# Kernel tuning notes

Hardware: AMD Instinct MI355X
Metric: run time of the kernel (lower is better)

## Reference

```python
import jax, jax.numpy as jnp
import numpy as np

B, NPTS = 2, 60000
NX, NY = 256, 256
PCR0, PCR1 = -32.0, -32.0
PS0, PS1 = 0.25, 0.25
MAXPP = 32      # max points per pillar
MAXP = 12000    # max pillars
C = 64          # lidar_channels
SENT = NX * NY  # sentinel pillar id (> any valid id)
NEG = -1e9
EPS = 1e-5


def setup_inputs():
    key = jax.random.key(0)
    ks = jax.random.split(key, 16)
    xy = jax.random.uniform(ks[0], (B, NPTS, 2), minval=-34.0, maxval=34.0)
    z = jax.random.uniform(ks[1], (B, NPTS, 1), minval=-3.0, maxval=1.0)
    ir = jax.random.uniform(ks[2], (B, NPTS, 2))
    pts = jnp.concatenate([xy, z, ir], axis=-1).astype(jnp.float32)
    mask = jax.random.uniform(ks[3], (B, NPTS)) < 0.98

    def lin(k, i, o):
        return (jax.random.normal(k, (i, o)) / np.sqrt(i)).astype(jnp.float32)

    inp = {"lidar_points": pts, "lidar_mask": mask,
           "w1": lin(ks[4], 10, 64), "b1": 0.01 * jax.random.normal(ks[5], (64,), jnp.float32),
           "g1": jnp.ones(64, jnp.float32), "be1": jnp.zeros(64, jnp.float32),
           "w2": lin(ks[6], 64, 64), "b2": 0.01 * jax.random.normal(ks[7], (64,), jnp.float32),
           "g2": jnp.ones(64, jnp.float32), "be2": jnp.zeros(64, jnp.float32)}
    for i, n in enumerate(["1", "2", "3"]):
        inp["cw" + n] = (jax.random.normal(ks[8 + i], (64, 64, 3, 3)) / np.sqrt(64 * 9)).astype(jnp.float32)
        inp["cb" + n] = 0.01 * jax.random.normal(ks[11 + i], (64,), jnp.float32)
        inp["cg" + n] = jnp.ones(64, jnp.float32)
        inp["cbe" + n] = jnp.zeros(64, jnp.float32)
    return inp


def bn1d(x, g, b):  # training-mode BN over rows (biased var), matches torch BatchNorm1d forward
    m = x.mean(0)
    v = ((x - m) ** 2).mean(0)
    return (x - m) * jax.lax.rsqrt(v + EPS) * g + b


def bn2d(x, g, b):  # training-mode BN over (N,H,W) per channel
    m = x.mean((0, 2, 3), keepdims=True)
    v = ((x - m) ** 2).mean((0, 2, 3), keepdims=True)
    return (x - m) * jax.lax.rsqrt(v + EPS) * g[None, :, None, None] + b[None, :, None, None]


def conv3(x, w, b):
    y = jax.lax.conv_general_dilated(x, w, (1, 1), 'SAME',
                                     dimension_numbers=('NCHW', 'OIHW', 'NCHW'))
    return y + b[None, :, None, None]


def pillarize(pts, msk):
    """pts: (N,5) xyzir, msk: (N,) bool -> padded pillar tensors (fixed shapes)."""
    n = pts.shape[0]
    ix = jnp.clip(((pts[:, 0] - PCR0) / PS0).astype(jnp.int32), 0, NX - 1)
    iy = jnp.clip(((pts[:, 1] - PCR1) / PS1).astype(jnp.int32), 0, NY - 1)
    pid = jnp.where(msk, iy * NX + ix, SENT)
    # sorted unique ids; keep the first (smallest) MAXP, like torch.unique + truncation
    spid = jnp.sort(pid)
    is_new = jnp.concatenate([jnp.array([True]), spid[1:] != spid[:-1]])
    urank = jnp.cumsum(is_new) - 1
    dest = jnp.where(is_new & (urank < MAXP) & (spid < SENT), urank, MAXP)
    uids = jnp.full((MAXP + 1,), SENT, dtype=pid.dtype).at[dest].set(spid)[:MAXP]  # ascending, SENT-padded
    inv = jnp.clip(jnp.searchsorted(uids, pid), 0, MAXP - 1)
    valid = (uids[inv] == pid) & (pid < SENT)
    # rank of each point within its pillar, in original point order (stable sort)
    seg = jnp.where(valid, inv, MAXP)
    order = jnp.argsort(seg)  # stable
    sseg = seg[order]
    pos = jnp.arange(n)
    first = jnp.concatenate([jnp.array([True]), sseg[1:] != sseg[:-1]])
    start = jax.lax.cummax(jnp.where(first, pos, 0))
    rank = jnp.zeros(n, jnp.int32).at[order].set((pos - start).astype(jnp.int32))
    keep = valid & (rank < MAXPP)  # first MAXPP points per pillar (matches truncation-then-mean)
    seg2 = jnp.where(keep, inv, MAXP)  # dump slot = MAXP
    cnt = jnp.zeros(MAXP + 1, pts.dtype).at[seg2].add(1.0)
    sums = jnp.zeros((MAXP + 1, 3), pts.dtype).at[seg2].add(jnp.where(keep[:, None], pts[:, :3], 0.0))
    mean = sums / jnp.maximum(cnt, 1.0)[:, None]
    ctr = mean[seg2]  # per-point pillar centroid (over kept points)
    gx = PCR0 + ((pid % NX).astype(pts.dtype) + 0.5) * PS0
    gy = PCR1 + ((pid // NX).astype(pts.dtype) + 0.5) * PS1
    aug = jnp.concatenate([pts, pts[:, :3] - ctr, gx[:, None], gy[:, None]], axis=1)  # (N,10)
    rk = jnp.minimum(rank, MAXPP - 1)
    pf = jnp.zeros((MAXP + 1, MAXPP, 10), pts.dtype).at[seg2, rk].set(
        jnp.where(keep[:, None], aug, 0.0))[:MAXP]
    pm = jnp.zeros((MAXP + 1, MAXPP), bool).at[seg2, rk].set(keep)[:MAXP]
    pvalid = uids < SENT
    coords = jnp.where(pvalid[:, None], jnp.stack([uids % NX, uids // NX], axis=-1), 0)
    return pf, pm, coords, pvalid


def pillar_net(pf, pm, w1, b1, g1, be1, w2, b2, g2, be2):
    npil, pp, ci = pf.shape
    x = pf.reshape(npil * pp, ci) @ w1 + b1
    x = jax.nn.relu(bn1d(x, g1, be1))
    x = x @ w2 + b2
    x = jax.nn.relu(bn1d(x, g2, be2))
    x = x.reshape(npil, pp, -1)
    x = jnp.where(pm[:, :, None], x, NEG)
    return x.max(axis=1)  # (npil, C)


def reference(lidar_points, lidar_mask, w1, b1, g1, be1, w2, b2, g2, be2,
              cw1, cb1, cg1, cbe1, cw2, cb2, cg2, cbe2, cw3, cb3, cg3, cbe3):
    pf, pm, coords, pvalid = jax.vmap(pillarize)(lidar_points, lidar_mask)
    # pillar net is applied per batch element in the original loop -> per-sample BN stats
    feat = jax.vmap(lambda a, m: pillar_net(a, m, w1, b1, g1, be1, w2, b2, g2, be2))(pf, pm)
    lin = coords[..., 1] * NX + coords[..., 0]          # (B, MAXP)
    f = jnp.where(pvalid[..., None], feat, 0.0)          # padded pillars contribute nothing
    bev = jax.vmap(lambda l, ff: jnp.zeros((NY * NX, C), ff.dtype).at[l].add(ff))(lin, f)
    bev = bev.reshape(-1, NY, NX, C).transpose(0, 3, 1, 2)  # (B,C,NY,NX)
    x = jax.nn.relu(bn2d(conv3(bev, cw1, cb1), cg1, cbe1))
    x = jax.nn.relu(bn2d(conv3(x, cw2, cb2), cg2, cbe2))
    x = jax.nn.relu(bn2d(conv3(x, cw3, cb3), cg3, cbe3))
    return x
```

## Files before the change

### kernel.cpp

```cpp
#include <hip/hip_runtime.h>

#define NPTS 60000
#define NXG 256
#define NCELL 65536
#define MAXP 12000
#define MAXPP 32
#define NROWS (MAXP*MAXPP)

typedef float f32x32 __attribute__((ext_vector_type(32)));
typedef float f32x4  __attribute__((ext_vector_type(4)));
typedef short s16x8  __attribute__((ext_vector_type(8)));

__device__ __forceinline__ short to_bf16(float f){
  unsigned u = __float_as_uint(f);
  unsigned r = (u + 0x7FFFu + ((u>>16)&1u)) >> 16;
  return (short)r;
}
__device__ __forceinline__ unsigned mapf(float f){
  unsigned u = __float_as_uint(f);
  return (u & 0x80000000u) ? ~u : (u | 0x80000000u);
}
__device__ __forceinline__ float unmapf(unsigned u){
  unsigned b = (u & 0x80000000u) ? (u ^ 0x80000000u) : ~u;
  return __uint_as_float(b);
}

__global__ __launch_bounds__(256) void prep(uint4* __restrict__ p1, size_t n1,
                                            uint4* __restrict__ p2, size_t n2,
                                            const float* __restrict__ w0, const float* __restrict__ w1,
                                            const float* __restrict__ w2, short* __restrict__ wh,
                                            const float* __restrict__ mw1, const float* __restrict__ mw2,
                                            short* __restrict__ w1h, short* __restrict__ w2h,
                                            uint4* __restrict__ fmn, size_t nfmn){
  size_t idx = (size_t)blockIdx.x*256 + threadIdx.x;
  size_t stride = (size_t)gridDim.x*256;
  const uint4 z = make_uint4(0,0,0,0);
  const uint4 ff = make_uint4(0xFFFFFFFFu,0xFFFFFFFFu,0xFFFFFFFFu,0xFFFFFFFFu);
  for (size_t k=idx; k<n1; k+=stride) p1[k]=z;
  for (size_t k=idx; k<n2; k+=stride) p2[k]=z;
  for (size_t k=idx; k<nfmn; k+=stride) fmn[k]=ff;
  for (size_t k=idx; k<3*36864; k+=stride){
    int l = (int)(k / 36864), r = (int)(k - (size_t)l*36864);
    const float* w = (l==0)? w0 : ((l==1)? w1 : w2);
    int ic = r & 63, oc = (r>>6)&63, tap = r>>12;
    wh[k] = to_bf16(w[(oc*64+ic)*9 + tap]);
  }
  for (size_t k=idx; k<2048; k+=stride){
    int kk = (int)(k>>6), oc = (int)(k&63);
    w1h[k] = (kk<10) ? to_bf16(mw1[kk*64+oc]) : (short)0;
  }
  for (size_t k=idx; k<4096; k+=stride)
    w2h[k] = to_bf16(mw2[k]);
}

__global__ void compute_pid(const float* __restrict__ pts, const void* __restrict__ maskp,
                            int* __restrict__ pid, int* __restrict__ ccnt){
  __shared__ int cf32, cbig;
  if (threadIdx.x==0){ cf32=0; cbig=0; }
  __syncthreads();
  {
    int lf=0, lb=0;
    const unsigned* mu = (const unsigned*)maskp;
    for (int k=0;k<4;k++){
      unsigned x = mu[threadIdx.x*4+k];
      if (x==0x3f800000u) lf++;
      else if (x>1u) lb++;
    }
    if (lf) atomicAdd(&cf32, lf);
    if (lb) atomicAdd(&cbig, lb);
  }
  __syncthreads();
  int mode = (cf32>64) ? 2 : ((cbig>0) ? 1 : 0);
  int i = blockIdx.x*blockDim.x + threadIdx.x;
  if (i>=NPTS) return;
  int b = blockIdx.y;
  int gi = b*NPTS+i;
  bool m;
  if (mode==0)      m = ((const int*)maskp)[gi]!=0;
  else if (mode==1) m = ((const unsigned char*)maskp)[gi]!=0;
  else              m = ((const float*)maskp)[gi]!=0.f;
  int cell = -1;
  if (m){
    float x = pts[(size_t)gi*5+0], y = pts[(size_t)gi*5+1];
    int ix = (int)((x - (-32.0f)) / 0.25f);
    ix = ix<0?0:(ix>255?255:ix);
    int iy = (int)((y - (-32.0f)) / 0.25f);
    iy = iy<0?0:(iy>255?255:iy);
    cell = iy*NXG + ix;
    atomicAdd(&ccnt[b*NCELL+cell], 1);
  }
  pid[gi] = cell;
}

__global__ __launch_bounds__(256) void scan_a(const int* __restrict__ ccnt,
                                              int2* __restrict__ bpart){
  int b = blockIdx.y, blk = blockIdx.x, t = threadIdx.x;
  int4 v = *(const int4*)&ccnt[b*NCELL + blk*1024 + t*4];
  int occ = (v.x>0)+(v.y>0)+(v.z>0)+(v.w>0);
  int cnt = v.x+v.y+v.z+v.w;
  #pragma unroll
  for (int off=32; off>0; off>>=1){
    occ += __shfl_xor(occ, off, 64);
    cnt += __shfl_xor(cnt, off, 64);
  }
  __shared__ int so[4], sc[4];
  int wv = t>>6, lane = t&63;
  if (lane==0){ so[wv]=occ; sc[wv]=cnt; }
  __syncthreads();
  if (t==0) bpart[b*64+blk] = make_int2(so[0]+so[1]+so[2]+so[3], sc[0]+sc[1]+sc[2]+sc[3]);
}

__global__ __launch_bounds__(256) void scan_b(const int* __restrict__ ccnt,
    const int2* __restrict__ bpart,
    int* __restrict__ crank, int* __restrict__ cstart, int* __restrict__ pcell,
    int* __restrict__ misc, int* __restrict__ heavy){
  __shared__ int swo[4], swc[4], sk[4];
  __shared__ int bo_, bc_;
  int b = blockIdx.y, blk = blockIdx.x, t = threadIdx.x;
  int wv = t>>6, lane = t&63;
  if (t < 64){
    int2 p = bpart[b*64+t];
    int po = (t<blk)? p.x : 0;
    int pc = (t<blk)? p.y : 0;
    int to = p.x;
    int tc = p.y;
    #pragma unroll
    for (int off=32; off>0; off>>=1){
      po += __shfl_xor(po, off, 64);
      pc += __shfl_xor(pc, off, 64);
      to += __shfl_xor(to, off, 64);
      tc += __shfl_xor(tc, off, 64);
    }
    if (t==0){
      bo_ = po; bc_ = pc;
      if (blk==0){
        misc[1+b] = (to < MAXP) ? to : MAXP;
        misc[5+b] = tc;
      }
    }
  }
  int4 v = *(const int4*)&ccnt[b*NCELL + blk*1024 + t*4];
  int occ = (v.x>0)+(v.y>0)+(v.z>0)+(v.w>0);
  int cnt = v.x+v.y+v.z+v.w;
  int io = occ, ic = cnt;
  #pragma unroll
  for (int off=1; off<64; off<<=1){
    int ao = __shfl_up(io, off, 64);
    int ac = __shfl_up(ic, off, 64);
    if (lane >= off){ io += ao; ic += ac; }
  }
  if (lane==63){ swo[wv]=io; swc[wv]=ic; }
  __syncthreads();
  int wvo=0, wvc=0;
  #pragma unroll
  for (int w2=0; w2<4; w2++){
    if (w2<wv){ wvo += swo[w2]; wvc += swc[w2]; }
  }
  int eo = bo_ + wvo + io - occ;
  int ec = bc_ + wvc + ic - cnt;
  int kept = 0;
  int cellb = blk*1024 + t*4;
  int vv[4] = {v.x,v.y,v.z,v.w};
  #pragma unroll
  for (int j=0;j<4;j++){
    int c = cellb+j; int val = vv[j];
    if (val>0){
      crank[b*NCELL+c]=eo; cstart[b*NCELL+c]=ec;
      if (eo<MAXP){
        pcell[b*MAXP+eo]=c;
        kept += (val<MAXPP)? val : MAXPP;
        if (val>MAXPP){
          int hi = atomicAdd(&heavy[b],1);
          if (hi<64) heavy[2 + b*64 + hi] = c;
        }
      }
      eo++; ec+=val;
    }
  }
  #pragma unroll
  for (int off=32; off>0; off>>=1) kept += __shfl_xor(kept, off, 64);
  if (lane==0) sk[wv]=kept;
  __syncthreads();
  if (t==0) atomicAdd(&misc[3+b], sk[0]+sk[1]+sk[2]+sk[3]);
}

__global__ void scatter_cpts(const float* __restrict__ pts, const int* __restrict__ pid,
    const int* __restrict__ ccnt, const int* __restrict__ crank, const int* __restrict__ cstart,
    int* __restrict__ ctmp, int* __restrict__ plist,
    float* __restrict__ cpts, float* __restrict__ psum){
  int i = blockIdx.x*blockDim.x + threadIdx.x;
  if (i>=NPTS) return;
  int b = blockIdx.y;
  int gi = b*NPTS+i;
  int cell = pid[gi];
  if (cell<0) return;
  int bc = b*NCELL+cell;
  int pos = cstart[bc] + atomicAdd(&ctmp[bc],1);
  plist[b*NPTS+pos] = i;
  int cnt = ccnt[bc], r = crank[bc];
  int rid = (r<MAXP && cnt<=MAXPP) ? r : -1;
  const float* qp = &pts[(size_t)gi*5];
  float x=qp[0], y=qp[1], z=qp[2], i1=qp[3], i2=qp[4];
  float gx = -32.0f + ((float)(cell&255)+0.5f)*0.25f;
  float gy = -32.0f + ((float)(cell>>8)+0.5f)*0.25f;
  float4* cp = (float4*)&cpts[(size_t)(b*NPTS+pos)*12];
  cp[0] = make_float4(x,y,z,i1);
  cp[1] = make_float4(i2,gx,gy,__int_as_float(rid));
  if (rid>=0){
    float* s = &psum[(size_t)(b*MAXP+rid)*4];
    atomicAdd(s+0,x); atomicAdd(s+1,y); atomicAdd(s+2,z); atomicAdd(s+3,1.f);
  }
}

__global__ void heavy_select(const float* __restrict__ pts,
    const int* __restrict__ ccnt, const int* __restrict__ crank,
    const int* __restrict__ cstart, const int* __restrict__ plist,
    const int* __restrict__ heavy, float* __restrict__ cpts, float* __restrict__ psum){
  int b = blockIdx.y;
  int hn = heavy[b]; if (hn>64) hn=64;
  if ((int)blockIdx.x >= hn) return;
  int cell = heavy[2 + b*64 + blockIdx.x];
  int bc = b*NCELL+cell;
  int cnt = ccnt[bc], start = cstart[bc], pr = crank[bc];
  for (int e=threadIdx.x; e<cnt; e+=blockDim.x){
    int pe = plist[b*NPTS+start+e];
    int rank=0;
    for (int k=0;k<cnt;k++) rank += (plist[b*NPTS+start+k] < pe);
    if (rank<MAXPP && pr<MAXP){
      cpts[(size_t)(b*NPTS+start+e)*12 + 7] = __int_as_float(pr);
      const float* qp = &pts[(size_t)(b*NPTS+pe)*5];
      float* s = &psum[(size_t)(b*MAXP+pr)*4];
      atomicAdd(s+0,qp[0]); atomicAdd(s+1,qp[1]); atomicAdd(s+2,qp[2]); atomicAdd(s+3,1.f);
    }
  }
}

#define MM_ACC(K,V) { if ((K)<32) m0[(K)&31]+=(V); else if ((K)<64) m1[((K)-32)&31]+=(V); else m2+=(V); }
__global__ __launch_bounds__(256) void moments(float* __restrict__ cpts,
    const float* __restrict__ psum, const int* __restrict__ misc,
    float* __restrict__ lstat){
  int b = blockIdx.y;
  int n = misc[5+b];
  f32x32 m0, m1; float m2 = 0.f;
  #pragma unroll
  for (int j=0;j<32;j++){ m0[j]=0.f; m1[j]=0.f; }
  for (int pos = blockIdx.x*256+threadIdx.x; pos<n; pos += gridDim.x*256){
    float4* cp = (float4*)&cpts[(size_t)(b*NPTS+pos)*12];
    float4 f1 = cp[0], f2 = cp[1];
    int rid = __float_as_int(f2.w);
    if (rid<0) continue;
    float4 mc = *(const float4*)&psum[(size_t)(b*MAXP+rid)*4];
    float inv = 1.f/fmaxf(mc.w,1.f);
    float dx = f1.x-mc.x*inv, dy = f1.y-mc.y*inv, dz = f1.z-mc.z*inv;
    cp[2] = make_float4(dx,dy,dz,0.f);
    float aug[10] = {f1.x,f1.y,f1.z,f1.w,f2.x, dx,dy,dz, f2.y,f2.z};
    #pragma unroll
    for (int d=0; d<10; d++){
      #pragma unroll
      for (int e=d; e<10; e++){
        const int k = d*10 - d*(d-1)/2 + (e-d);
        MM_ACC(k, aug[d]*aug[e]);
      }
      const int kl = 55+d;
      MM_ACC(kl, aug[d]);
    }
  }
  int lane = threadIdx.x & 63;
  int rep = ((blockIdx.x*256+threadIdx.x)>>6) & 15;
  float* dst = &lstat[(size_t)(rep*2+b)*65];
  #pragma unroll
  for (int j=0;j<32;j++){
    float v = m0[j];
    #pragma unroll
    for (int off=32; off>0; off>>=1) v += __shfl_xor(v, off, 64);
    if (lane==0) atomicAdd(&dst[j], v);
  }
  #pragma unroll
  for (int j=0;j<32;j++){
    float v = m1[j];
    #pragma unroll
    for (int off=32; off>0; off>>=1) v += __shfl_xor(v, off, 64);
    if (lane==0) atomicAdd(&dst[32+j], v);
  }
  {
    float v = m2;
    #pragma unroll
    for (int off=32; off>0; off>>=1) v += __shfl_xor(v, off, 64);
    if (lane==0) atomicAdd(&dst[64], v);
  }
}

#define MFMA16(A,B,C) __builtin_amdgcn_mfma_f32_16x16x32_bf16(A,B,C,0,0,0)

__global__ __launch_bounds__(256) void point_mlp(const float* __restrict__ cpts,
    const int* __restrict__ misc,
    const float* __restrict__ w1, const float* __restrict__ b1,
    const float* __restrict__ g1, const float* __restrict__ be1,
    const short* __restrict__ w1h, const short* __restrict__ w2h,
    const float* __restrict__ lstat, float* __restrict__ l2stat,
    unsigned* __restrict__ fmxU, unsigned* __restrict__ fmnU){
  __shared__ float sM[65];
  __shared__ float sBN1[128];
  __shared__ short zT[4][16*72];
  const int b = blockIdx.y;
  const int t = threadIdx.x;
  for (int e=t; e<65; e+=256){
    float s=0.f;
    for (int r=0;r<16;r++) s += lstat[(size_t)(r*2+b)*65+e];
    sM[e]=s;
  }
  __syncthreads();
  if (t < 64){
    int c = t;
    float wcol[10];
    #pragma unroll
    for (int d=0;d<10;d++) wcol[d] = w1[d*64+c];
    float b1c = b1[c];
    float nk = (float)misc[3+b];
    const float N = (float)NROWS;
    float pad = N - nk;
    float lw = 0.f;
    #pragma unroll
    for (int d=0;d<10;d++) lw += sM[55+d]*wcol[d];
    float s = nk*b1c + lw;
    float qq = nk*b1c*b1c + 2.f*b1c*lw;
    #pragma unroll
    for (int d=0; d<10; d++){
      #pragma unroll
      for (int e=d; e<10; e++){
        float m = sM[d*10 - d*(d-1)/2 + (e-d)];
        qq += ((d==e)?1.f:2.f)*m*wcol[d]*wcol[e];
      }
    }
    float St = s + pad*b1c;
    float Qt = qq + pad*b1c*b1c;
    float mu = St/N;
    float var = fmaxf(Qt/N - mu*mu, 0.f);
    float sc = g1[c]*rsqrtf(var+1e-5f);
    float sh = be1[c]-mu*sc;
    sBN1[c]=sc; sBN1[64+c]=b1c*sc+sh;
  }
  __syncthreads();
  const int lane = t & 63, wv = t >> 6;
  const int colx = lane & 15;
  const int kq = lane >> 4, kb = kq*8;
  s16x8 w1f0, w1f1, w1f2, w1f3;
  s16x8 a2f0, a2f1, a2f2, a2f3;
  s16x8 b2f0, b2f1, b2f2, b2f3;
  #pragma unroll
  for (int j=0;j<8;j++){
    w1f0[j]=w1h[(kb+j)*64 +  0+colx]; w1f1[j]=w1h[(kb+j)*64 + 16+colx];
    w1f2[j]=w1h[(kb+j)*64 + 32+colx]; w1f3[j]=w1h[(kb+j)*64 + 48+colx];
    a2f0[j]=w2h[(kb+j)*64 +  0+colx]; a2f1[j]=w2h[(kb+j)*64 + 16+colx];
    a2f2[j]=w2h[(kb+j)*64 + 32+colx]; a2f3[j]=w2h[(kb+j)*64 + 48+colx];
    b2f0[j]=w2h[(32+kb+j)*64 +  0+colx]; b2f1[j]=w2h[(32+kb+j)*64 + 16+colx];
    b2f2[j]=w2h[(32+kb+j)*64 + 32+colx]; b2f3[j]=w2h[(32+kb+j)*64 + 48+colx];
  }
  float sc1v0=sBN1[colx],    sh1v0=sBN1[64+colx];
  float sc1v1=sBN1[16+colx], sh1v1=sBN1[80+colx];
  float sc1v2=sBN1[32+colx], sh1v2=sBN1[96+colx];
  float sc1v3=sBN1[48+colx], sh1v3=sBN1[112+colx];
  const int n = misc[5+b];
  const int ntiles = (n+15)>>4;
  short* myZ = zT[wv];
  f32x4 s24={0.f,0.f,0.f,0.f}, q24=s24;
  for (int tile = blockIdx.x*4 + wv; tile < ntiles; tile += gridDim.x*4){
    int pos0 = tile*16;
    int pos = pos0 + colx;
    float aug[10];
    #pragma unroll
    for (int d=0;d<10;d++) aug[d]=0.f;
    if (pos < n){
      const float4* cp = (const float4*)&cpts[(size_t)(b*NPTS+pos)*12];
      float4 f1 = cp[0], f2 = cp[1], f3 = cp[2];
      aug[0]=f1.x; aug[1]=f1.y; aug[2]=f1.z; aug[3]=f1.w; aug[4]=f2.x;
      aug[5]=f3.x; aug[6]=f3.y; aug[7]=f3.z;
      aug[8]=f2.y; aug[9]=f2.z;
    }
    s16x8 af;
    #pragma unroll
    for (int j=0;j<8;j++){
      float v = 0.f;
      if (kq==0) v = aug[j];
      else if (kq==1 && j<2) v = aug[8+j];
      af[j] = to_bf16(v);
    }
    f32x4 y0={0.f,0.f,0.f,0.f}, y1=y0, y2=y0, y3=y0;
    y0 = MFMA16(af, w1f0, y0);
    y1 = MFMA16(af, w1f1, y1);
    y2 = MFMA16(af, w1f2, y2);
    y3 = MFMA16(af, w1f3, y3);
    #pragma unroll
    for (int m=0;m<4;m++){
      int pr = (kq*4+m)*72;
      myZ[pr +  0+colx] = to_bf16(fmaxf(y0[m]*sc1v0+sh1v0, 0.f));
      myZ[pr + 16+colx] = to_bf16(fmaxf(y1[m]*sc1v1+sh1v1, 0.f));
      myZ[pr + 32+colx] = to_bf16(fmaxf(y2[m]*sc1v2+sh1v2, 0.f));
      myZ[pr + 48+colx] = to_bf16(fmaxf(y3[m]*sc1v3+sh1v3, 0.f));
    }
    s16x8 az0 = *(const s16x8*)&myZ[colx*72 + kb];
    s16x8 az1 = *(const s16x8*)&myZ[colx*72 + 32 + kb];
    f32x4 t0={0.f,0.f,0.f,0.f}, t1=t0, t2=t0, t3=t0;
    t0 = MFMA16(az0, a2f0, t0); t0 = MFMA16(az1, b2f0, t0);
    t1 = MFMA16(az0, a2f1, t1); t1 = MFMA16(az1, b2f1, t1);
    t2 = MFMA16(az0, a2f2, t2); t2 = MFMA16(az1, b2f2, t2);
    t3 = MFMA16(az0, a2f3, t3); t3 = MFMA16(az1, b2f3, t3);
    int cur = -1;
    f32x4 tmx={-1e30f,-1e30f,-1e30f,-1e30f}, tmn={1e30f,1e30f,1e30f,1e30f};
    #pragma unroll
    for (int m=0;m<4;m++){
      int pm = pos0 + kq*4 + m;
      int rid = -1;
      if (pm < n) rid = __float_as_int(cpts[(size_t)(b*NPTS+pm)*12 + 7]);
      if (rid != cur){
        if (cur >= 0){
          size_t base = (size_t)(b*MAXP+cur)*64;
          atomicMax(&fmxU[base+ 0+colx], mapf(tmx[0]));
          atomicMax(&fmxU[base+16+colx], mapf(tmx[1]));
          atomicMax(&fmxU[base+32+colx], mapf(tmx[2]));
          atomicMax(&fmxU[base+48+colx], mapf(tmx[3]));
          atomicMin(&fmnU[base+ 0+colx], mapf(tmn[0]));
          atomicMin(&fmnU[base+16+colx], mapf(tmn[1]));
          atomicMin(&fmnU[base+32+colx], mapf(tmn[2]));
          atomicMin(&fmnU[base+48+colx], mapf(tmn[3]));
        }
        cur = rid;
        tmx[0]=-1e30f; tmx[1]=-1e30f; tmx[2]=-1e30f; tmx[3]=-1e30f;
        tmn[0]= 1e30f; tmn[1]= 1e30f; tmn[2]= 1e30f; tmn[3]= 1e30f;
      }
      if (rid >= 0){
        float v0=t0[m], v1=t1[m], v2=t2[m], v3=t3[m];
        tmx[0]=fmaxf(tmx[0],v0); tmn[0]=fminf(tmn[0],v0);
        tmx[1]=fmaxf(tmx[1],v1); tmn[1]=fminf(tmn[1],v1);
        tmx[2]=fmaxf(tmx[2],v2); tmn[2]=fminf(tmn[2],v2);
        tmx[3]=fmaxf(tmx[3],v3); tmn[3]=fminf(tmn[3],v3);
        s24[0]+=v0; q24[0]+=v0*v0;
        s24[1]+=v1; q24[1]+=v1*v1;
        s24[2]+=v2; q24[2]+=v2*v2;
        s24[3]+=v3; q24[3]+=v3*v3;
      }
    }
    if (cur >= 0){
      size_t base = (size_t)(b*MAXP+cur)*64;
      atomicMax(&fmxU[base+ 0+colx], mapf(tmx[0]));
      atomicMax(&fmxU[base+16+colx], mapf(tmx[1]));
      atomicMax(&fmxU[base+32+colx], mapf(tmx[2]));
      atomicMax(&fmxU[base+48+colx], mapf(tmx[3]));
      atomicMin(&fmnU[base+ 0+colx], mapf(tmn[0]));
      atomicMin(&fmnU[base+16+colx], mapf(tmn[1]));
      atomicMin(&fmnU[base+32+colx], mapf(tmn[2]));
      atomicMin(&fmnU[base+48+colx], mapf(tmn[3]));
    }
  }
  int rep = (blockIdx.x*4 + wv) & 15;
  float* L = &l2stat[(size_t)((rep*2+b)*2+0)*64];
  atomicAdd(&L[ 0+colx], s24[0]);
  atomicAdd(&L[16+colx], s24[1]);
  atomicAdd(&L[32+colx], s24[2]);
  atomicAdd(&L[48+colx], s24[3]);
  float* Q = &l2stat[(size_t)((rep*2+b)*2+1)*64];
  atomicAdd(&Q[ 0+colx], q24[0]);
  atomicAdd(&Q[16+colx], q24[1]);
  atomicAdd(&Q[32+colx], q24[2]);
  atomicAdd(&Q[48+colx], q24[3]);
}

__global__ __launch_bounds__(256) void scatter_bev(
    const float* __restrict__ w1, const float* __restrict__ b1,
    const float* __restrict__ g1, const float* __restrict__ be1,
    const float* __restrict__ w2, const float* __restrict__ b2,
    const float* __restrict__ g2, const float* __restrict__ be2,
    const float* __restrict__ lstat, const float* __restrict__ l2stat,
    const unsigned* __restrict__ fmxU, const unsigned* __restrict__ fmnU,
    const int* __restrict__ pcell, const int* __restrict__ misc,
    short* __restrict__ bevh){
  __shared__ float M[65];
  __shared__ float z0s[64];
  __shared__ float sBN2[128];
  const int b = blockIdx.y;
  for (int e=threadIdx.x; e<65; e+=256){
    float s=0.f;
    for (int r=0;r<16;r++) s += lstat[(size_t)(r*2+b)*65+e];
    M[e]=s;
  }
  __syncthreads();
  if (threadIdx.x < 64){
    int c = threadIdx.x;
    float wcol[10];
    #pragma unroll
    for (int d=0;d<10;d++) wcol[d] = w1[d*64+c];
    float b1c = b1[c];
    float nk = (float)misc[3+b];
    const float N = (float)NROWS;
    float pad = N - nk;
    float lw = 0.f;
    #pragma unroll
    for (int d=0;d<10;d++) lw += M[55+d]*wcol[d];
    float s = nk*b1c + lw;
    float qq = nk*b1c*b1c + 2.f*b1c*lw;
    #pragma unroll
    for (int d=0; d<10; d++){
      #pragma unroll
      for (int e=d; e<10; e++){
        float m = M[d*10 - d*(d-1)/2 + (e-d)];
        qq += ((d==e)?1.f:2.f)*m*wcol[d]*wcol[e];
      }
    }
    float St = s + pad*b1c;
    float Qt = qq + pad*b1c*b1c;
    float mu = St/N;
    float var = fmaxf(Qt/N - mu*mu, 0.f);
    float sc1 = g1[c]*rsqrtf(var+1e-5f);
    float sh1 = be1[c]-mu*sc1;
    z0s[c] = fmaxf(b1c*sc1+sh1, 0.f);
  }
  __syncthreads();
  if (threadIdx.x < 64){
    int c = threadIdx.x;
    float nk = (float)misc[3+b];
    const float N = (float)NROWS;
    float pad = N - nk;
    float t0 = b2[c];
    for (int i2=0;i2<64;i2++) t0 += z0s[i2]*w2[(size_t)i2*64+c];
    float s2 = pad*t0, q2 = pad*t0*t0;
    for (int r=0;r<16;r++){
      s2 += l2stat[(size_t)((r*2+b)*2+0)*64+c];
      q2 += l2stat[(size_t)((r*2+b)*2+1)*64+c];
    }
    float m2 = s2/N;
    float v2 = fmaxf(q2/N - m2*m2, 0.f);
    float sc2 = g2[c]*rsqrtf(v2+1e-5f);
    sBN2[c]=sc2; sBN2[64+c]=be2[c]-m2*sc2;
  }
  __syncthreads();
  const int npil = misc[1+b];
  for (int tid = blockIdx.x*256+threadIdx.x; tid < 64*MAXP; tid += gridDim.x*256){
    int c = tid & 63;
    int p = tid >> 6;
    if (p >= npil) break;
    float sc2 = sBN2[c], sh2 = sBN2[64+c];
    size_t idx = (size_t)(b*MAXP+p)*64 + c;
    float tv = (sc2 >= 0.f) ? unmapf(fmxU[idx]) : unmapf(fmnU[idx]);
    float v = fmaxf(sc2*tv+sh2, 0.f);
    int cell = pcell[b*MAXP+p];
    bevh[((size_t)((b<<16) + cell))*64 + c] = to_bf16(v);
  }
}

__global__ __launch_bounds__(512,4) void conv_mfma(const short* __restrict__ xh,
    const short* __restrict__ wh, const float* __restrict__ bias,
    const float* __restrict__ pstat, const float* __restrict__ pg, const float* __restrict__ pbe,
    short* __restrict__ outh, float* __restrict__ outf,
    float* __restrict__ stat){
  __shared__ short sX[324*40];
  __shared__ short sW[576*40];
  __shared__ float sBN[128];
  __shared__ float ss[64], sq[64];
  const int tX = blockIdx.x*16, tY = blockIdx.y*16;
  const int b = blockIdx.z;
  const int t = threadIdx.x;
  const int lane = t & 63, wv = t >> 6;
  const int colx = lane & 15;
  const int kb = (lane >> 4) * 8;
  const int ocb = (wv >> 2) * 32;
  const int ry  = (wv & 3) * 4;
  if (t < 64){ ss[t]=0.f; sq[t]=0.f; }
  if (t >= 64 && t < 128 && pstat){
    int c = t-64;
    const float n = 131072.f;
    float m = pstat[c]/n;
    float v = fmaxf(pstat[64+c]/n - m*m, 0.f);
    float sc = pg[c]*rsqrtf(v+1e-5f);
    sBN[c]=sc; sBN[64+c]=pbe[c]-m*sc;
  }

  f32x4 a00={0.f,0.f,0.f,0.f}, a01=a00, a02=a00, a03=a00;
  f32x4 a10=a00, a11=a00, a12=a00, a13=a00;

  for (int h=0; h<2; ++h){
    __syncthreads();
    for (int e=t; e<1296; e+=512){
      int px = e>>2, j = e&3;
      int yy = px/18, xx = px - yy*18;
      int gy = tY+yy-1, gx = tX+xx-1;
      uint4 v = make_uint4(0,0,0,0);
      if ((unsigned)gy<256u && (unsigned)gx<256u){
        v = *(const uint4*)&xh[((size_t)((b<<16) + (gy<<8) + gx))*64 + h*32 + j*8];
        if (pstat){
          unsigned arr[4] = {v.x, v.y, v.z, v.w};
          #pragma unroll
          for (int j2=0;j2<4;j2++){
            unsigned wrd = arr[j2];
            int ch = h*32 + j*8 + j2*2;
            float lo = __uint_as_float(wrd<<16);
            float hi = __uint_as_float(wrd & 0xffff0000u);
            lo = fmaxf(lo*sBN[ch]+sBN[64+ch], 0.f);
            hi = fmaxf(hi*sBN[ch+1]+sBN[64+ch+1], 0.f);
            arr[j2] = (unsigned)(unsigned short)to_bf16(lo) |
                      (((unsigned)(unsigned short)to_bf16(hi))<<16);
          }
          v = make_uint4(arr[0],arr[1],arr[2],arr[3]);
        }
      }
      *(uint4*)&sX[px*40 + j*8] = v;
    }
    for (int e=t; e<2304; e+=512){
      int row = e>>2, j = e&3;
      int tap = row>>6, oc = row&63;
      uint4 v = *(const uint4*)&wh[(size_t)tap*4096 + oc*64 + h*32 + j*8];
      *(uint4*)&sW[row*40 + j*8] = v;
    }
    __syncthreads();
    #pragma unroll
    for (int tap=0; tap<9; ++tap){
      const int dy = tap/3, dx = tap - dy*3;
      s16x8 wA = *(const s16x8*)&sW[(tap*64 + ocb +  0 + colx)*40 + kb];
      s16x8 wB = *(const s16x8*)&sW[(tap*64 + ocb + 16 + colx)*40 + kb];
      s16x8 x0 = *(const s16x8*)&sX[((ry+0+dy)*18 + colx+dx)*40 + kb];
      s16x8 x1 = *(const s16x8*)&sX[((ry+1+dy)*18 + colx+dx)*40 + kb];
      s16x8 x2 = *(const s16x8*)&sX[((ry+2+dy)*18 + colx+dx)*40 + kb];
      s16x8 x3 = *(const s16x8*)&sX[((ry+3+dy)*18 + colx+dx)*40 + kb];
      a00 = MFMA16(wA,x0,a00); a01 = MFMA16(wA,x1,a01);
      a02 = MFMA16(wA,x2,a02); a03 = MFMA16(wA,x3,a03);
      a10 = MFMA16(wB,x0,a10); a11 = MFMA16(wB,x1,a11);
      a12 = MFMA16(wB,x2,a12); a13 = MFMA16(wB,x3,a13);
    }
  }
  const int ocl = (lane>>4)*4;
  #define DOG(G, A0,A1,A2,A3) { \
    const int oc0g = ocb + G*16 + ocl; \
    float bj0=bias[oc0g], bj1=bias[oc0g+1], bj2=bias[oc0g+2], bj3=bias[oc0g+3]; \
    float v00=A0[0]+bj0, v01=A0[1]+bj1, v02=A0[2]+bj2, v03=A0[3]+bj3; \
    float v10=A1[0]+bj0, v11=A1[1]+bj1, v12=A1[2]+bj2, v13=A1[3]+bj3; \
    float v20=A2[0]+bj0, v21=A2[1]+bj1, v22=A2[2]+bj2, v23=A2[3]+bj3; \
    float v30=A3[0]+bj0, v31=A3[1]+bj1, v32=A3[2]+bj2, v33=A3[3]+bj3; \
    float s0=v00+v10+v20+v30, q0=v00*v00+v10*v10+v20*v20+v30*v30; \
    float s1=v01+v11+v21+v31, q1=v01*v01+v11*v11+v21*v21+v31*v31; \
    float s2=v02+v12+v22+v32, q2=v02*v02+v12*v12+v22*v22+v32*v32; \
    float s3=v03+v13+v23+v33, q3=v03*v03+v13*v13+v23*v23+v33*v33; \
    s0+=__shfl_xor(s0,1,64); s0+=__shfl_xor(s0,2,64); s0+=__shfl_xor(s0,4,64); s0+=__shfl_xor(s0,8,64); \
    q0+=__shfl_xor(q0,1,64); q0+=__shfl_xor(q0,2,64); q0+=__shfl_xor(q0,4,64); q0+=__shfl_xor(q0,8,64); \
    s1+=__shfl_xor(s1,1,64); s1+=__shfl_xor(s1,2,64); s1+=__shfl_xor(s1,4,64); s1+=__shfl_xor(s1,8,64); \
    q1+=__shfl_xor(q1,1,64); q1+=__shfl_xor(q1,2,64); q1+=__shfl_xor(q1,4,64); q1+=__shfl_xor(q1,8,64); \
    s2+=__shfl_xor(s2,1,64); s2+=__shfl_xor(s2,2,64); s2+=__shfl_xor(s2,4,64); s2+=__shfl_xor(s2,8,64); \
    q2+=__shfl_xor(q2,1,64); q2+=__shfl_xor(q2,2,64); q2+=__shfl_xor(q2,4,64); q2+=__shfl_xor(q2,8,64); \
    s3+=__shfl_xor(s3,1,64); s3+=__shfl_xor(s3,2,64); s3+=__shfl_xor(s3,4,64); s3+=__shfl_xor(s3,8,64); \
    q3+=__shfl_xor(q3,1,64); q3+=__shfl_xor(q3,2,64); q3+=__shfl_xor(q3,4,64); q3+=__shfl_xor(q3,8,64); \
    if (colx==0){ \
      atomicAdd(&ss[oc0g],s0);   atomicAdd(&sq[oc0g],q0); \
      atomicAdd(&ss[oc0g+1],s1); atomicAdd(&sq[oc0g+1],q1); \
      atomicAdd(&ss[oc0g+2],s2); atomicAdd(&sq[oc0g+2],q2); \
      atomicAdd(&ss[oc0g+3],s3); atomicAdd(&sq[oc0g+3],q3); \
    } \
    if (outh){ \
      size_t pb = (size_t)((b<<16) + tX + colx); \
      *(short4*)&outh[(pb + ((tY+ry+0)<<8))*64 + oc0g] = make_short4(to_bf16(v00),to_bf16(v01),to_bf16(v02),to_bf16(v03)); \
      *(short4*)&outh[(pb + ((tY+ry+1)<<8))*64 + oc0g] = make_short4(to_bf16(v10),to_bf16(v11),to_bf16(v12),to_bf16(v13)); \
      *(short4*)&outh[(pb + ((tY+ry+2)<<8))*64 + oc0g] = make_short4(to_bf16(v20),to_bf16(v21),to_bf16(v22),to_bf16(v23)); \
      *(short4*)&outh[(pb + ((tY+ry+3)<<8))*64 + oc0g] = make_short4(to_bf16(v30),to_bf16(v31),to_bf16(v32),to_bf16(v33)); \
    } else { \
      size_t cb0 = (((size_t)(b*64+oc0g))<<16) + ((tY+ry)<<8) + tX + colx; \
      outf[cb0          ] = v00; outf[cb0+(1<<16)      ] = v01; outf[cb0+(2<<16)      ] = v02; outf[cb0+(3<<16)      ] = v03; \
      outf[cb0+256      ] = v10; outf[cb0+(1<<16)+256  ] = v11; outf[cb0+(2<<16)+256  ] = v12; outf[cb0+(3<<16)+256  ] = v13; \
      outf[cb0+512      ] = v20; outf[cb0+(1<<16)+512  ] = v21; outf[cb0+(2<<16)+512  ] = v22; outf[cb0+(3<<16)+512  ] = v23; \
      outf[cb0+768      ] = v30; outf[cb0+(1<<16)+768  ] = v31; outf[cb0+(2<<16)+768  ] = v32; outf[cb0+(3<<16)+768  ] = v33; \
    } \
  }
  DOG(0, a00,a01,a02,a03)
  DOG(1, a10,a11,a12,a13)
  #undef DOG
  __syncthreads();
  if (t < 64){
    atomicAdd(&stat[t],    ss[t]);
    atomicAdd(&stat[64+t], sq[t]);
  }
}

__global__ __launch_bounds__(256) void bn_apply(float* __restrict__ x, const float* __restrict__ bnst,
                                                const float* __restrict__ g, const float* __restrict__ be){
  __shared__ float sBN[128];
  if (threadIdx.x < 64){
    int c = threadIdx.x;
    const float n = 131072.f;
    float m = bnst[c]/n;
    float v = fmaxf(bnst[64+c]/n - m*m, 0.f);
    float sc = g[c]*rsqrtf(v+1e-5f);
    sBN[c]=sc; sBN[64+c]=be[c]-m*sc;
  }
  __syncthreads();
  size_t idx = (size_t)blockIdx.x*256 + threadIdx.x;
  size_t stride = (size_t)gridDim.x*256;
  float4* p = (float4*)x;
  for (size_t k=idx; k<2097152ULL; k+=stride){
    int c = (int)((k>>14)&63);
    float sc = sBN[c], sh = sBN[64+c];
    float4 v = p[k];
    v.x=fmaxf(v.x*sc+sh,0.f); v.y=fmaxf(v.y*sc+sh,0.f);
    v.z=fmaxf(v.z*sc+sh,0.f); v.w=fmaxf(v.w*sc+sh,0.f);
    p[k]=v;
  }
}

extern "C" void kernel_launch(void* const* d_in, const int* in_sizes, int n_in,
                              void* d_out, int out_size, void* d_ws, size_t ws_size,
                              hipStream_t stream){
  const float* pts  = (const float*)d_in[0];
  const void*  mask = d_in[1];
  const float* w1 = (const float*)d_in[2];
  const float* b1 = (const float*)d_in[3];
  const float* g1 = (const float*)d_in[4];
  const float* be1= (const float*)d_in[5];
  const float* w2 = (const float*)d_in[6];
  const float* b2 = (const float*)d_in[7];
  const float* g2 = (const float*)d_in[8];
  const float* be2= (const float*)d_in[9];
  const float* cw[3]  = {(const float*)d_in[10],(const float*)d_in[14],(const float*)d_in[18]};
  const float* cb[3]  = {(const float*)d_in[11],(const float*)d_in[15],(const float*)d_in[19]};
  const float* cg[3]  = {(const float*)d_in[12],(const float*)d_in[16],(const float*)d_in[20]};
  const float* cbe[3] = {(const float*)d_in[13],(const float*)d_in[17],(const float*)d_in[21]};
  float* out = (float*)d_out;

  char* W = (char*)d_ws;
  size_t off = 0;
  auto A = [&](size_t n){ size_t r = off; off = (off + n + 255) & ~(size_t)255; return r; };
  short*    BIGH  = (short*)   (W + A((size_t)2*NCELL*64*2));
  short*    OUT1H = (short*)   (W + A((size_t)2*NCELL*64*2));
  int*      PID   = (int*)     (W + A((size_t)2*NPTS*4));
  int*      CRANK = (int*)     (W + A((size_t)2*NCELL*4));
  int*      CSTART= (int*)     (W + A((size_t)2*NCELL*4));
  int*      PLIST = (int*)     (W + A((size_t)2*NPTS*4));
  int*      PCELL = (int*)     (W + A((size_t)2*MAXP*4));
  float*    CPTS  = (float*)   (W + A((size_t)2*NPTS*12*4));
  unsigned* FMN   = (unsigned*)(W + A((size_t)2*MAXP*64*4));
  short*    WH    = (short*)   (W + A((size_t)3*36864*2));
  short*    W1H   = (short*)   (W + A((size_t)2048*2));
  short*    W2H   = (short*)   (W + A((size_t)4096*2));
  int2*     BPART = (int2*)    (W + A((size_t)2*64*8));
  size_t zbeg = off;
  unsigned* FMX   = (unsigned*)(W + A((size_t)2*MAXP*64*4));
  int*      CCNT  = (int*)     (W + A((size_t)2*NCELL*4));
  int*      CTMP  = (int*)     (W + A((size_t)2*NCELL*4));
  float*    PSUM  = (float*)   (W + A((size_t)2*MAXP*16));
  float*    LSTAT = (float*)   (W + A((size_t)16*2*65*4));
  float*    L2STAT= (float*)   (W + A((size_t)16*2*2*64*4));
  float*    BNST  = (float*)   (W + A((size_t)3*256*4));
  int*      HEAVY = (int*)     (W + A((size_t)(2+2*64)*4));
  int*      MISC  = (int*)     (W + A(256));
  size_t zend = off;

  prep<<<2048,256,0,stream>>>((uint4*)BIGH, (size_t)2*NCELL*64*2/16,
                              (uint4*)(W+zbeg), (zend-zbeg)/16,
                              cw[0], cw[1], cw[2], WH, w1, w2, W1H, W2H,
                              (uint4*)FMN, (size_t)2*MAXP*64*4/16);

  dim3 perPt((NPTS+255)/256, 2);

  compute_pid<<<perPt,256,0,stream>>>(pts, mask, PID, CCNT);
  scan_a<<<dim3(64,2),256,0,stream>>>(CCNT, BPART);
  scan_b<<<dim3(64,2),256,0,stream>>>(CCNT, BPART, CRANK, CSTART, PCELL, MISC, HEAVY);
  scatter_cpts<<<perPt,256,0,stream>>>(pts, PID, CCNT, CRANK, CSTART, CTMP, PLIST, CPTS, PSUM);
  heavy_select<<<dim3(64,2),64,0,stream>>>(pts, CCNT, CRANK, CSTART, PLIST, HEAVY, CPTS, PSUM);
  moments<<<dim3(120,2),256,0,stream>>>(CPTS, PSUM, MISC, LSTAT);
  point_mlp<<<dim3(256,2),256,0,stream>>>(CPTS, MISC, w1, b1, g1, be1,
                                          W1H, W2H, LSTAT, L2STAT, FMX, FMN);
  scatter_bev<<<dim3(512,2),256,0,stream>>>(w1, b1, g1, be1, w2, b2, g2, be2,
                                            LSTAT, L2STAT, FMX, FMN, PCELL, MISC, BIGH);

  conv_mfma<<<dim3(16,16,2),512,0,stream>>>(BIGH, WH, cb[0], nullptr, nullptr, nullptr,
                                            OUT1H, nullptr, BNST);
  conv_mfma<<<dim3(16,16,2),512,0,stream>>>(OUT1H, WH+36864, cb[1], BNST, cg[0], cbe[0],
                                            BIGH, nullptr, BNST+256);
  conv_mfma<<<dim3(16,16,2),512,0,stream>>>(BIGH, WH+2*36864, cb[2], BNST+256, cg[1], cbe[1],
                                            nullptr, out, BNST+512);
  bn_apply<<<2048,256,0,stream>>>(out, BNST+512, cg[2], cbe[2]);
}
```

Baseline: 226.6 us.

## Split point MLP segmented max/min reduction into separate kernel via buffer

The point MLP kernel now writes its per-point second-layer outputs to a new global buffer instead of doing the per-pillar max/min atomics and BN statistics inline. A new seg_max kernel reads that buffer with one lane per channel, runs the segmented max/min over 16-point chunks, and accumulates the sum and sum-of-squares statistics. This is meant to take atomic contention and divergent control flow out of the MFMA loop. In exchange it adds about 30 MB of global round-trip traffic and one more kernel launch.

```diff
diff --git a/kernel.cpp b/kernel.cpp
--- a/kernel.cpp
+++ b/kernel.cpp
@@ -297,8 +297,7 @@
     const float* __restrict__ w1, const float* __restrict__ b1,
     const float* __restrict__ g1, const float* __restrict__ be1,
     const short* __restrict__ w1h, const short* __restrict__ w2h,
-    const float* __restrict__ lstat, float* __restrict__ l2stat,
-    unsigned* __restrict__ fmxU, unsigned* __restrict__ fmnU){
+    const float* __restrict__ lstat, float* __restrict__ tbuf){
   __shared__ float sM[65];
   __shared__ float sBN1[128];
   __shared__ short zT[4][16*72];
@@ -363,7 +362,6 @@
   const int n = misc[5+b];
   const int ntiles = (n+15)>>4;
   short* myZ = zT[wv];
-  f32x4 s24={0.f,0.f,0.f,0.f}, q24=s24;
   for (int tile = blockIdx.x*4 + wv; tile < ntiles; tile += gridDim.x*4){
     int pos0 = tile*16;
     int pos = pos0 + colx;
@@ -405,64 +403,57 @@
     t1 = MFMA16(az0, a2f1, t1); t1 = MFMA16(az1, b2f1, t1);
     t2 = MFMA16(az0, a2f2, t2); t2 = MFMA16(az1, b2f2, t2);
     t3 = MFMA16(az0, a2f3, t3); t3 = MFMA16(az1, b2f3, t3);
-    int cur = -1;
-    f32x4 tmx={-1e30f,-1e30f,-1e30f,-1e30f}, tmn={1e30f,1e30f,1e30f,1e30f};
     #pragma unroll
     for (int m=0;m<4;m++){
       int pm = pos0 + kq*4 + m;
-      int rid = -1;
-      if (pm < n) rid = __float_as_int(cpts[(size_t)(b*NPTS+pm)*12 + 7]);
-      if (rid != cur){
-        if (cur >= 0){
-          size_t base = (size_t)(b*MAXP+cur)*64;
-          atomicMax(&fmxU[base+ 0+colx], mapf(tmx[0]));
-          atomicMax(&fmxU[base+16+colx], mapf(tmx[1]));
-          atomicMax(&fmxU[base+32+colx], mapf(tmx[2]));
-          atomicMax(&fmxU[base+48+colx], mapf(tmx[3]));
-          atomicMin(&fmnU[base+ 0+colx], mapf(tmn[0]));
-          atomicMin(&fmnU[base+16+colx], mapf(tmn[1]));
-          atomicMin(&fmnU[base+32+colx], mapf(tmn[2]));
-          atomicMin(&fmnU[base+48+colx], mapf(tmn[3]));
+      if (pm < n){
+        float* dst = &tbuf[(size_t)(b*NPTS+pm)*64];
+        dst[ 0+colx] = t0[m];
+        dst[16+colx] = t1[m];
+        dst[32+colx] = t2[m];
+        dst[48+colx] = t3[m];
+      }
+    }
+  }
+}
+
+__global__ __launch_bounds__(256) void seg_max(const float* __restrict__ tbuf,
+    const float* __restrict__ cpts, const int* __restrict__ misc,
+    float* __restrict__ l2stat, unsigned* __restrict__ fmxU, unsigned* __restrict__ fmnU){
+  const int b = blockIdx.y;
+  const int lane = threadIdx.x & 63;
+  const int n = misc[5+b];
+  const int w = blockIdx.x*4 + (threadIdx.x>>6);
+  float s2 = 0.f, q2 = 0.f;
+  int p0 = w*16;
+  if (p0 < n){
+    int p1 = p0+16; if (p1>n) p1=n;
+    int cur = -1;
+    float tmax = -1e30f, tmin = 1e30f;
+    for (int pos=p0; pos<p1; ++pos){
+      int rid = __float_as_int(cpts[(size_t)(b*NPTS+pos)*12 + 7]);
+      float tv = tbuf[(size_t)(b*NPTS+pos)*64 + lane];
+      if (rid >= 0){
+        if (rid != cur){
+          if (cur >= 0){
+            atomicMax(&fmxU[(size_t)(b*MAXP+cur)*64 + lane], mapf(tmax));
+            atomicMin(&fmnU[(size_t)(b*MAXP+cur)*64 + lane], mapf(tmin));
+          }
+          cur = rid; tmax = -1e30f; tmin = 1e30f;
         }
-        cur = rid;
-        tmx[0]=-1e30f; tmx[1]=-1e30f; tmx[2]=-1e30f; tmx[3]=-1e30f;
-        tmn[0]= 1e30f; tmn[1]= 1e30f; tmn[2]= 1e30f; tmn[3]= 1e30f;
+        tmax = fmaxf(tmax, tv);
+        tmin = fminf(tmin, tv);
+        s2 += tv; q2 += tv*tv;
       }
-      if (rid >= 0){
-        float v0=t0[m], v1=t1[m], v2=t2[m], v3=t3[m];
-        tmx[0]=fmaxf(tmx[0],v0); tmn[0]=fminf(tmn[0],v0);
-        tmx[1]=fmaxf(tmx[1],v1); tmn[1]=fminf(tmn[1],v1);
-        tmx[2]=fmaxf(tmx[2],v2); tmn[2]=fminf(tmn[2],v2);
-        tmx[3]=fmaxf(tmx[3],v3); tmn[3]=fminf(tmn[3],v3);
-        s24[0]+=v0; q24[0]+=v0*v0;
-        s24[1]+=v1; q24[1]+=v1*v1;
-        s24[2]+=v2; q24[2]+=v2*v2;
-        s24[3]+=v3; q24[3]+=v3*v3;
-      }
     }
     if (cur >= 0){
-      size_t base = (size_t)(b*MAXP+cur)*64;
-      atomicMax(&fmxU[base+ 0+colx], mapf(tmx[0]));
-      atomicMax(&fmxU[base+16+colx], mapf(tmx[1]));
-      atomicMax(&fmxU[base+32+colx], mapf(tmx[2]));
-      atomicMax(&fmxU[base+48+colx], mapf(tmx[3]));
-      atomicMin(&fmnU[base+ 0+colx], mapf(tmn[0]));
-      atomicMin(&fmnU[base+16+colx], mapf(tmn[1]));
-      atomicMin(&fmnU[base+32+colx], mapf(tmn[2]));
-      atomicMin(&fmnU[base+48+colx], mapf(tmn[3]));
-    }
-  }
-  int rep = (blockIdx.x*4 + wv) & 15;
-  float* L = &l2stat[(size_t)((rep*2+b)*2+0)*64];
-  atomicAdd(&L[ 0+colx], s24[0]);
-  atomicAdd(&L[16+colx], s24[1]);
-  atomicAdd(&L[32+colx], s24[2]);
-  atomicAdd(&L[48+colx], s24[3]);
-  float* Q = &l2stat[(size_t)((rep*2+b)*2+1)*64];
-  atomicAdd(&Q[ 0+colx], q24[0]);
-  atomicAdd(&Q[16+colx], q24[1]);
-  atomicAdd(&Q[32+colx], q24[2]);
-  atomicAdd(&Q[48+colx], q24[3]);
+      atomicMax(&fmxU[(size_t)(b*MAXP+cur)*64 + lane], mapf(tmax));
+      atomicMin(&fmnU[(size_t)(b*MAXP+cur)*64 + lane], mapf(tmin));
+    }
+  }
+  int rep = w & 15;
+  atomicAdd(&l2stat[(size_t)((rep*2+b)*2+0)*64+lane], s2);
+  atomicAdd(&l2stat[(size_t)((rep*2+b)*2+1)*64+lane], q2);
 }
 
 __global__ __launch_bounds__(256) void scatter_bev(
@@ -731,6 +722,7 @@
   int*      PLIST = (int*)     (W + A((size_t)2*NPTS*4));
   int*      PCELL = (int*)     (W + A((size_t)2*MAXP*4));
   float*    CPTS  = (float*)   (W + A((size_t)2*NPTS*12*4));
+  float*    TBUF  = (float*)   (W + A((size_t)2*NPTS*64*4));
   unsigned* FMN   = (unsigned*)(W + A((size_t)2*MAXP*64*4));
   short*    WH    = (short*)   (W + A((size_t)3*36864*2));
   short*    W1H   = (short*)   (W + A((size_t)2048*2));
@@ -762,7 +754,8 @@
   heavy_select<<<dim3(64,2),64,0,stream>>>(pts, CCNT, CRANK, CSTART, PLIST, HEAVY, CPTS, PSUM);
   moments<<<dim3(120,2),256,0,stream>>>(CPTS, PSUM, MISC, LSTAT);
   point_mlp<<<dim3(256,2),256,0,stream>>>(CPTS, MISC, w1, b1, g1, be1,
-                                          W1H, W2H, LSTAT, L2STAT, FMX, FMN);
+                                          W1H, W2H, LSTAT, TBUF);
+  seg_max<<<dim3(938,2),256,0,stream>>>(TBUF, CPTS, MISC, L2STAT, FMX, FMN);
   scatter_bev<<<dim3(512,2),256,0,stream>>>(w1, b1, g1, be1, w2, b2, g2, be2,
                                             LSTAT, L2STAT, FMX, FMN, PCELL, MISC, BIGH);
 
```

Measured after the change: 215.7 us, median of 2. -4.8%, faster.
